# Kernel optimization log

Measured on AMD Instinct MI355X. Metric: run time of the kernel, lower is better.

Reference implementation:

```python
import jax, jax.numpy as jnp
import numpy as np

N = 50000       # nodes
E = 800000      # edges (before self-loops)
F_IN = 128      # num_features
HID = 32        # hidden_dim per head
HEADS = 8
C = 40          # num_classes
NEG_SLOPE = 0.2 # PyG GATConv default leaky_relu slope


def setup_inputs() -> dict:
    key = jax.random.key(0)
    ks = jax.random.split(key, 10)
    x = jax.random.normal(ks[0], (N, F_IN), jnp.float32)
    edge_index = jax.random.randint(ks[1], (2, E), 0, N, dtype=jnp.int64)
    W1 = jax.random.normal(ks[2], (F_IN, HEADS * HID), jnp.float32) * np.float32(1.0 / np.sqrt(F_IN))
    a1_src = jax.random.normal(ks[3], (HEADS, HID), jnp.float32) * 0.1
    a1_dst = jax.random.normal(ks[4], (HEADS, HID), jnp.float32) * 0.1
    b1 = jnp.zeros((HEADS * HID,), jnp.float32)
    W2 = jax.random.normal(ks[5], (HEADS * HID, C), jnp.float32) * np.float32(1.0 / np.sqrt(HEADS * HID))
    a2_src = jax.random.normal(ks[6], (1, C), jnp.float32) * 0.1
    a2_dst = jax.random.normal(ks[7], (1, C), jnp.float32) * 0.1
    b2 = jnp.zeros((C,), jnp.float32)
    return {"x": x, "edge_index": edge_index,
            "W1": W1, "a1_src": a1_src, "a1_dst": a1_dst, "b1": b1,
            "W2": W2, "a2_src": a2_src, "a2_dst": a2_dst, "b2": b2}


def gat_conv(x, edge_index, W, a_src, a_dst, bias):
    """PyG-style GATConv (concat heads, add_self_loops=True), inference mode (no dropout)."""
    n = x.shape[0]
    heads, out_dim = a_src.shape
    ar = jnp.arange(n, dtype=edge_index.dtype)
    src = jnp.concatenate([edge_index[0], ar])   # [E+N]
    dst = jnp.concatenate([edge_index[1], ar])   # [E+N]
    h = (x @ W).reshape(n, heads, out_dim)       # [N, H, D]
    alpha_src = jnp.einsum('nhd,hd->nh', h, a_src)  # [N, H]
    alpha_dst = jnp.einsum('nhd,hd->nh', h, a_dst)  # [N, H]
    e = jax.nn.leaky_relu(alpha_src[src] + alpha_dst[dst], NEG_SLOPE)  # [E+N, H]
    # segment softmax over edges grouped by destination node
    m = jax.ops.segment_max(e, dst, num_segments=n)          # [N, H]
    ex = jnp.exp(e - m[dst])                                  # [E+N, H]
    s = jax.ops.segment_sum(ex, dst, num_segments=n)          # [N, H]
    alpha = ex / (s[dst] + 1e-16)                              # [E+N, H]
    msg = h[src] * alpha[..., None]                            # [E+N, H, D]
    out = jax.ops.segment_sum(msg, dst, num_segments=n)       # [N, H, D]
    return out.reshape(n, heads * out_dim) + bias


def reference(x, edge_index, W1, a1_src, a1_dst, b1, W2, a2_src, a2_dst, b2):
    h = jax.nn.elu(gat_conv(x, edge_index, W1, a1_src, a1_dst, b1))
    # F.dropout is identity in eval mode
    return gat_conv(h, edge_index, W2, a2_src, a2_dst, b2)
```

## Files before the change

kernel.cpp:

```cpp
#include <hip/hip_runtime.h>
#include <math.h>

#define F_IN 128
#define HID 32
#define HEADS 8
#define HD 256
#define NC 40
#define NCP 48
#define H2S 64
#define NEG 0.2f

typedef _Float16 half8 __attribute__((ext_vector_type(8)));
typedef _Float16 half4v __attribute__((ext_vector_type(4)));
typedef float f32x4 __attribute__((ext_vector_type(4)));

__device__ __forceinline__ float leaky(float v) { return v > 0.0f ? v : NEG * v; }
__device__ __forceinline__ float2 up2(unsigned int u) {
    union { unsigned int u; _Float16 h[2]; } c; c.u = u;
    return make_float2((float)c.h[0], (float)c.h[1]);
}

__global__ __launch_bounds__(256) void prep_count_k(const float* __restrict__ W1,
        const float* __restrict__ W2, const float* __restrict__ a1s,
        const float* __restrict__ a1d, _Float16* __restrict__ W1t,
        _Float16* __restrict__ W2t, _Float16* __restrict__ Pt,
        const int* __restrict__ ei, int* __restrict__ deg,
        int* __restrict__ ord, int E) {
    int i = blockIdx.x * 256 + threadIdx.x;
    if (i < HD * F_IN) {
        int c = i >> 7, k = i & 127;
        W1t[i] = (_Float16)W1[k * HD + c];
    }
    int j = i - HD * F_IN;
    if (j >= 0 && j < NCP * HD) {
        int c = j >> 8, k = j & 255;
        W2t[j] = (c < NC) ? (_Float16)W2[k * NC + c] : (_Float16)0.0f;
    }
    int e = i - (HD * F_IN + NCP * HD);
    if (e >= 0 && e < E) {
        int dst = ei[E + e];
        ord[e] = atomicAdd(&deg[dst], 1);
    }
    int p = i - (HD * F_IN + NCP * HD + E);
    if (p >= 0 && p < 16 * F_IN) {
        int pj = p >> 7, k = p & 127;
        int h = pj & 7;
        const float* av = (pj < 8) ? (a1s + h * HID) : (a1d + h * HID);
        const float* wr = W1 + (size_t)k * HD + h * HID;
        float acc = 0.0f;
#pragma unroll 8
        for (int d = 0; d < HID; ++d) acc = fmaf(wr[d], av[d], acc);
        Pt[pj * F_IN + k] = (_Float16)acc;
    }
}

__global__ __launch_bounds__(256) void scan1_k(const int* __restrict__ deg,
        int* __restrict__ rowptr, int* __restrict__ partial, int N) {
    __shared__ int tmp[256];
    int t = threadIdx.x;
    int idx = blockIdx.x * 256 + t;
    int v = (idx < N) ? (deg[idx] + 1) : 0;
    tmp[t] = v;
    __syncthreads();
#pragma unroll
    for (int off = 1; off < 256; off <<= 1) {
        int add = (t >= off) ? tmp[t - off] : 0;
        __syncthreads();
        tmp[t] += add;
        __syncthreads();
    }
    if (idx < N) rowptr[idx] = tmp[t] - v;
    if (t == 255) partial[blockIdx.x] = tmp[255];
}

__global__ __launch_bounds__(256) void scan2_k(int* __restrict__ partial, int P) {
    __shared__ int tmp[256];
    int t = threadIdx.x;
    int v = (t < P) ? partial[t] : 0;
    tmp[t] = v;
    __syncthreads();
#pragma unroll
    for (int off = 1; off < 256; off <<= 1) {
        int add = (t >= off) ? tmp[t - off] : 0;
        __syncthreads();
        tmp[t] += add;
        __syncthreads();
    }
    if (t < P) partial[t] = tmp[t] - v;
}

__global__ __launch_bounds__(256) void scan3_k(int* __restrict__ rowptr,
        const int* __restrict__ partial, int* __restrict__ esrc, int N, int EN) {
    int idx = blockIdx.x * 256 + threadIdx.x;
    if (idx >= N) return;
    int rp = rowptr[idx] + partial[blockIdx.x];
    rowptr[idx] = rp;
    esrc[rp] = idx;
    if (idx == 0) rowptr[N] = EN;
}

__global__ __launch_bounds__(256) void scatter_k(const int* __restrict__ ei,
        const int* __restrict__ rowptr, const int* __restrict__ ord,
        int* __restrict__ esrc, int E) {
    int e = blockIdx.x * 256 + threadIdx.x;
    if (e >= E) return;
    int src = ei[e], dst = ei[E + e];
    esrc[rowptr[dst] + 1 + ord[e]] = src;
}

__global__ __launch_bounds__(256) void gemm1_k(const float* __restrict__ x,
        const _Float16* __restrict__ W1t, const _Float16* __restrict__ Pt,
        _Float16* __restrict__ H1, float* __restrict__ asrc,
        float* __restrict__ adst, int N) {
    int t = threadIdx.x;
    int w = t >> 6, l = t & 63;
    int quad = l >> 4, lr = l & 15;
    int rowA = blockIdx.x * 64 + w * 16 + lr;
    int rowL = rowA < N ? rowA : N - 1;

    half8 af[4];
    const float* xr = x + (size_t)rowL * F_IN + quad * 8;
#pragma unroll
    for (int s = 0; s < 4; ++s) {
        float4 u = *(const float4*)(xr + s * 32);
        float4 v = *(const float4*)(xr + s * 32 + 4);
        half8 a;
        a[0] = (_Float16)u.x; a[1] = (_Float16)u.y;
        a[2] = (_Float16)u.z; a[3] = (_Float16)u.w;
        a[4] = (_Float16)v.x; a[5] = (_Float16)v.y;
        a[6] = (_Float16)v.z; a[7] = (_Float16)v.w;
        af[s] = a;
    }

    int rowC0 = blockIdx.x * 64 + w * 16 + quad * 4;
#pragma unroll
    for (int tt = 0; tt < 16; ++tt) {
        f32x4 acc = {0.0f, 0.0f, 0.0f, 0.0f};
        const _Float16* wp = W1t + (size_t)(tt * 16 + lr) * F_IN + quad * 8;
#pragma unroll
        for (int s = 0; s < 4; ++s) {
            half8 b = *(const half8*)(wp + s * 32);
            acc = __builtin_amdgcn_mfma_f32_16x16x32_f16(af[s], b, acc, 0, 0, 0);
        }
#pragma unroll
        for (int r = 0; r < 4; ++r) {
            int rr = rowC0 + r;
            if (rr < N) H1[(size_t)rr * HD + tt * 16 + lr] = (_Float16)acc[r];
        }
    }
    {
        f32x4 acc = {0.0f, 0.0f, 0.0f, 0.0f};
        const _Float16* pp = Pt + (size_t)lr * F_IN + quad * 8;
#pragma unroll
        for (int s = 0; s < 4; ++s) {
            half8 b = *(const half8*)(pp + s * 32);
            acc = __builtin_amdgcn_mfma_f32_16x16x32_f16(af[s], b, acc, 0, 0, 0);
        }
#pragma unroll
        for (int r = 0; r < 4; ++r) {
            int rr = rowC0 + r;
            if (rr < N) {
                if (lr < 8) asrc[rr * HEADS + lr] = acc[r];
                else        adst[rr * HEADS + (lr - 8)] = acc[r];
            }
        }
    }
}

__global__ __launch_bounds__(256) void agg1_k(const int* __restrict__ esrc,
        const int* __restrict__ rowptr, const float* __restrict__ asrc,
        const float* __restrict__ adst, const _Float16* __restrict__ H1,
        const float* __restrict__ b1, _Float16* __restrict__ out1, int N) {
    int t = threadIdx.x;
    int lane = t & 63;
    int dst = blockIdx.x * 4 + (t >> 6);
    if (dst >= N) return;
    int j = lane & 7;
    int h = lane >> 3;
    int start = rowptr[dst], end = rowptr[dst + 1];
    float adh = adst[dst * HEADS + h];

    float s = 0.0f;
    for (int e = start + j; e < end; e += 8)
        s += __expf(leaky(asrc[esrc[e] * HEADS + h] + adh));
    s += __shfl_xor(s, 1, 64);
    s += __shfl_xor(s, 2, 64);
    s += __shfl_xor(s, 4, 64);
    float inv = 1.0f / (s + 1e-16f);

    float a0 = 0.0f, a1 = 0.0f, a2 = 0.0f, a3 = 0.0f;
    int e = start;
    for (; e + 7 < end; e += 8) {
        int si[8]; float al[8]; uint2 hv[8];
#pragma unroll
        for (int q = 0; q < 8; ++q) si[q] = esrc[e + q];
#pragma unroll
        for (int q = 0; q < 8; ++q) {
            al[q] = asrc[si[q] * HEADS + h];
            hv[q] = *(const uint2*)(H1 + (size_t)si[q] * HD + lane * 4);
        }
#pragma unroll
        for (int q = 0; q < 8; ++q) {
            float w = __expf(leaky(al[q] + adh)) * inv;
            float2 p0 = up2(hv[q].x), p1 = up2(hv[q].y);
            a0 = fmaf(p0.x, w, a0); a1 = fmaf(p0.y, w, a1);
            a2 = fmaf(p1.x, w, a2); a3 = fmaf(p1.y, w, a3);
        }
    }
    for (; e + 3 < end; e += 4) {
        int si[4]; float al[4]; uint2 hv[4];
#pragma unroll
        for (int q = 0; q < 4; ++q) si[q] = esrc[e + q];
#pragma unroll
        for (int q = 0; q < 4; ++q) {
            al[q] = asrc[si[q] * HEADS + h];
            hv[q] = *(const uint2*)(H1 + (size_t)si[q] * HD + lane * 4);
        }
#pragma unroll
        for (int q = 0; q < 4; ++q) {
            float w = __expf(leaky(al[q] + adh)) * inv;
            float2 p0 = up2(hv[q].x), p1 = up2(hv[q].y);
            a0 = fmaf(p0.x, w, a0); a1 = fmaf(p0.y, w, a1);
            a2 = fmaf(p1.x, w, a2); a3 = fmaf(p1.y, w, a3);
        }
    }
    for (; e < end; ++e) {
        int s0 = esrc[e];
        float al0 = asrc[s0 * HEADS + h];
        uint2 h0 = *(const uint2*)(H1 + (size_t)s0 * HD + lane * 4);
        float w0 = __expf(leaky(al0 + adh)) * inv;
        float2 p0 = up2(h0.x), p1 = up2(h0.y);
        a0 = fmaf(p0.x, w0, a0); a1 = fmaf(p0.y, w0, a1);
        a2 = fmaf(p1.x, w0, a2); a3 = fmaf(p1.y, w0, a3);
    }
    float4 bv = *(const float4*)(b1 + lane * 4);
    float o0 = a0 + bv.x, o1 = a1 + bv.y, o2 = a2 + bv.z, o3 = a3 + bv.w;
    o0 = o0 > 0.0f ? o0 : expm1f(o0);
    o1 = o1 > 0.0f ? o1 : expm1f(o1);
    o2 = o2 > 0.0f ? o2 : expm1f(o2);
    o3 = o3 > 0.0f ? o3 : expm1f(o3);
    half4v o;
    o[0] = (_Float16)o0; o[1] = (_Float16)o1;
    o[2] = (_Float16)o2; o[3] = (_Float16)o3;
    *(half4v*)(out1 + (size_t)dst * HD + lane * 4) = o;
}

__global__ __launch_bounds__(256) void gemm2_k(const _Float16* __restrict__ out1,
        const _Float16* __restrict__ W2t, const float* __restrict__ a2s,
        const float* __restrict__ a2d, _Float16* __restrict__ H2h,
        float* __restrict__ asrc2, float* __restrict__ adst2, int N) {
    int t = threadIdx.x;
    int w = t >> 6, l = t & 63;
    int quad = l >> 4, lr = l & 15;
    int rowA = blockIdx.x * 64 + w * 16 + lr;
    int rowL = rowA < N ? rowA : N - 1;

    half8 af[8];
    const _Float16* ar = out1 + (size_t)rowL * HD + quad * 8;
#pragma unroll
    for (int s = 0; s < 8; ++s) af[s] = *(const half8*)(ar + s * 32);

    f32x4 acc[3];
#pragma unroll
    for (int tt = 0; tt < 3; ++tt) {
        f32x4 a = {0.0f, 0.0f, 0.0f, 0.0f};
        const _Float16* wp = W2t + (size_t)(tt * 16 + lr) * HD + quad * 8;
#pragma unroll
        for (int s = 0; s < 8; ++s) {
            half8 b = *(const half8*)(wp + s * 32);
            a = __builtin_amdgcn_mfma_f32_16x16x32_f16(af[s], b, a, 0, 0, 0);
        }
        acc[tt] = a;
    }

    float a2sv[3], a2dv[3];
#pragma unroll
    for (int tt = 0; tt < 3; ++tt) {
        int col = tt * 16 + lr;
        a2sv[tt] = (col < NC) ? a2s[col] : 0.0f;
        a2dv[tt] = (col < NC) ? a2d[col] : 0.0f;
    }
    int rowC0 = blockIdx.x * 64 + w * 16 + quad * 4;
#pragma unroll
    for (int r = 0; r < 4; ++r) {
        int row = rowC0 + r;
        if (row >= N) break;
        float ps = 0.0f, pd = 0.0f;
#pragma unroll
        for (int tt = 0; tt < 3; ++tt) {
            int col = tt * 16 + lr;
            float v = acc[tt][r];
            H2h[(size_t)row * H2S + col] = (_Float16)v;
            ps = fmaf(v, a2sv[tt], ps);
            pd = fmaf(v, a2dv[tt], pd);
        }
        ps += __shfl_xor(ps, 1, 64); ps += __shfl_xor(ps, 2, 64);
        ps += __shfl_xor(ps, 4, 64); ps += __shfl_xor(ps, 8, 64);
        pd += __shfl_xor(pd, 1, 64); pd += __shfl_xor(pd, 2, 64);
        pd += __shfl_xor(pd, 4, 64); pd += __shfl_xor(pd, 8, 64);
        if (lr == 0) { asrc2[row] = ps; adst2[row] = pd; }
    }
}

__global__ __launch_bounds__(256) void agg2_k(const int* __restrict__ esrc,
        const int* __restrict__ rowptr, const float* __restrict__ asrc,
        const float* __restrict__ adst, const _Float16* __restrict__ H2h,
        const float* __restrict__ b2, float* __restrict__ dout, int N) {
    int t = threadIdx.x;
    int g = t >> 6, lane = t & 63;
    int dst = blockIdx.x * 4 + g;
    if (dst >= N) return;
    int start = rowptr[dst], end = rowptr[dst + 1];
    float adst_v = adst[dst];

    float sloc = 0.0f;
    for (int e = start + lane; e < end; e += 64)
        sloc += __expf(leaky(asrc[esrc[e]] + adst_v));
#pragma unroll
    for (int off = 32; off > 0; off >>= 1)
        sloc += __shfl_xor(sloc, off, 64);
    float inv = 1.0f / (sloc + 1e-16f);

    float acc = 0.0f;
    int e = start;
    for (; e + 3 < end; e += 4) {
        int s0 = esrc[e], s1 = esrc[e + 1], s2 = esrc[e + 2], s3 = esrc[e + 3];
        float al0 = asrc[s0], al1 = asrc[s1], al2 = asrc[s2], al3 = asrc[s3];
        float v0 = (float)H2h[(size_t)s0 * H2S + lane];
        float v1 = (float)H2h[(size_t)s1 * H2S + lane];
        float v2 = (float)H2h[(size_t)s2 * H2S + lane];
        float v3 = (float)H2h[(size_t)s3 * H2S + lane];
        float w0 = __expf(leaky(al0 + adst_v)) * inv;
        float w1 = __expf(leaky(al1 + adst_v)) * inv;
        float w2 = __expf(leaky(al2 + adst_v)) * inv;
        float w3 = __expf(leaky(al3 + adst_v)) * inv;
        acc = fmaf(v0, w0, acc);
        acc = fmaf(v1, w1, acc);
        acc = fmaf(v2, w2, acc);
        acc = fmaf(v3, w3, acc);
    }
    for (; e < end; ++e) {
        int s0 = esrc[e];
        float w0 = __expf(leaky(asrc[s0] + adst_v)) * inv;
        acc = fmaf((float)H2h[(size_t)s0 * H2S + lane], w0, acc);
    }
    if (lane < NC) dout[(size_t)dst * NC + lane] = acc + b2[lane];
}

extern "C" void kernel_launch(void* const* d_in, const int* in_sizes, int n_in,
                              void* d_out, int out_size, void* d_ws, size_t ws_size,
                              hipStream_t stream) {
    const float* x   = (const float*)d_in[0];
    const int*   ei  = (const int*)d_in[1];
    const float* W1  = (const float*)d_in[2];
    const float* a1s = (const float*)d_in[3];
    const float* a1d = (const float*)d_in[4];
    const float* b1  = (const float*)d_in[5];
    const float* W2  = (const float*)d_in[6];
    const float* a2s = (const float*)d_in[7];
    const float* a2d = (const float*)d_in[8];
    const float* b2  = (const float*)d_in[9];
    float* dout = (float*)d_out;

    int N = in_sizes[0] / F_IN;
    int E = in_sizes[1] / 2;
    int EN = E + N;
    int NB = (N + 255) / 256;

    char* base = (char*)d_ws;
    size_t off = 0;
    auto carve = [&](size_t bytes) { char* p = base + off; off += (bytes + 255) & ~(size_t)255; return p; };
    _Float16* H1   = (_Float16*)carve((size_t)N * HD * 2);
    _Float16* W1t  = (_Float16*)carve((size_t)HD * F_IN * 2);
    _Float16* W2t  = (_Float16*)carve((size_t)NCP * HD * 2);
    _Float16* Pt   = (_Float16*)carve((size_t)16 * F_IN * 2);
    _Float16* out1 = (_Float16*)carve((size_t)N * HD * 2);
    _Float16* H2h  = (_Float16*)carve((size_t)N * H2S * 2);
    float* asrc1  = (float*)carve((size_t)N * HEADS * 4);
    float* adst1  = (float*)carve((size_t)N * HEADS * 4);
    float* asrc2  = (float*)carve((size_t)N * 4);
    float* adst2  = (float*)carve((size_t)N * 4);
    int*   deg    = (int*)carve((size_t)N * 4);
    int*   ord    = (int*)carve((size_t)E * 4);
    int*   rowptr = (int*)carve((size_t)(N + 1) * 4);
    int*   part   = (int*)carve((size_t)NB * 4);
    int*   esrc   = (int*)carve((size_t)EN * 4);

    hipMemsetAsync(deg, 0, (size_t)N * 4, stream);
    int prep_total = HD * F_IN + NCP * HD + E + 16 * F_IN;
    hipLaunchKernelGGL(prep_count_k, dim3((prep_total + 255) / 256), dim3(256), 0, stream,
                       W1, W2, a1s, a1d, W1t, W2t, Pt, ei, deg, ord, E);
    hipLaunchKernelGGL(scan1_k, dim3(NB), dim3(256), 0, stream, deg, rowptr, part, N);
    hipLaunchKernelGGL(scan2_k, dim3(1), dim3(256), 0, stream, part, NB);
    hipLaunchKernelGGL(scan3_k, dim3(NB), dim3(256), 0, stream, rowptr, part, esrc, N, EN);
    hipLaunchKernelGGL(scatter_k, dim3((E + 255) / 256), dim3(256), 0, stream, ei, rowptr, ord, esrc, E);

    hipLaunchKernelGGL(gemm1_k, dim3((N + 63) / 64), dim3(256), 0, stream,
                       x, W1t, Pt, H1, asrc1, adst1, N);
    hipLaunchKernelGGL(agg1_k, dim3((N + 3) / 4), dim3(256), 0, stream,
                       esrc, rowptr, asrc1, adst1, H1, b1, out1, N);

    hipLaunchKernelGGL(gemm2_k, dim3((N + 63) / 64), dim3(256), 0, stream,
                       out1, W2t, a2s, a2d, H2h, asrc2, adst2, N);
    hipLaunchKernelGGL(agg2_k, dim3((N + 3) / 4), dim3(256), 0, stream,
                       esrc, rowptr, asrc2, adst2, H2h, b2, dout, N);
}
```

Baseline: 316.6 us.

## Fuse softmax denominator into aggregation pass and merge scan kernels

Both aggregation kernels now accumulate the softmax denominator during the single gather pass and normalize once at the end. This removes the separate pass that re-read edge indices and source scores. The second and third scan kernels are merged: every block redundantly scans the partial sums in shared memory, which saves one launch. Layer 2 aggregation also gains an 8-way unrolled gather loop to expose more memory-level parallelism, at the cost of more registers.

```diff
diff --git a/kernel.cpp b/kernel.cpp
--- a/kernel.cpp
+++ b/kernel.cpp
@@ -73,29 +73,27 @@
     if (t == 255) partial[blockIdx.x] = tmp[255];
 }
 
-__global__ __launch_bounds__(256) void scan2_k(int* __restrict__ partial, int P) {
-    __shared__ int tmp[256];
-    int t = threadIdx.x;
-    int v = (t < P) ? partial[t] : 0;
-    tmp[t] = v;
+__global__ __launch_bounds__(256) void scan23_k(int* __restrict__ rowptr,
+        const int* __restrict__ partial, int* __restrict__ esrc,
+        int N, int EN, int NB) {
+    __shared__ int ps[256];
+    int t = threadIdx.x;
+    ps[t] = (t < NB) ? partial[t] : 0;
     __syncthreads();
 #pragma unroll
     for (int off = 1; off < 256; off <<= 1) {
-        int add = (t >= off) ? tmp[t - off] : 0;
+        int add = (t >= off) ? ps[t - off] : 0;
         __syncthreads();
-        tmp[t] += add;
+        ps[t] += add;
         __syncthreads();
     }
-    if (t < P) partial[t] = tmp[t] - v;
-}
-
-__global__ __launch_bounds__(256) void scan3_k(int* __restrict__ rowptr,
-        const int* __restrict__ partial, int* __restrict__ esrc, int N, int EN) {
-    int idx = blockIdx.x * 256 + threadIdx.x;
-    if (idx >= N) return;
-    int rp = rowptr[idx] + partial[blockIdx.x];
-    rowptr[idx] = rp;
-    esrc[rp] = idx;
+    int base = (blockIdx.x == 0) ? 0 : ps[blockIdx.x - 1];
+    int idx = blockIdx.x * 256 + t;
+    if (idx < N) {
+        int rp = rowptr[idx] + base;
+        rowptr[idx] = rp;
+        esrc[rp] = idx;
+    }
     if (idx == 0) rowptr[N] = EN;
 }
 
@@ -175,19 +173,11 @@
     int lane = t & 63;
     int dst = blockIdx.x * 4 + (t >> 6);
     if (dst >= N) return;
-    int j = lane & 7;
     int h = lane >> 3;
     int start = rowptr[dst], end = rowptr[dst + 1];
     float adh = adst[dst * HEADS + h];
 
     float s = 0.0f;
-    for (int e = start + j; e < end; e += 8)
-        s += __expf(leaky(asrc[esrc[e] * HEADS + h] + adh));
-    s += __shfl_xor(s, 1, 64);
-    s += __shfl_xor(s, 2, 64);
-    s += __shfl_xor(s, 4, 64);
-    float inv = 1.0f / (s + 1e-16f);
-
     float a0 = 0.0f, a1 = 0.0f, a2 = 0.0f, a3 = 0.0f;
     int e = start;
     for (; e + 7 < end; e += 8) {
@@ -201,7 +191,8 @@
         }
 #pragma unroll
         for (int q = 0; q < 8; ++q) {
-            float w = __expf(leaky(al[q] + adh)) * inv;
+            float w = __expf(leaky(al[q] + adh));
+            s += w;
             float2 p0 = up2(hv[q].x), p1 = up2(hv[q].y);
             a0 = fmaf(p0.x, w, a0); a1 = fmaf(p0.y, w, a1);
             a2 = fmaf(p1.x, w, a2); a3 = fmaf(p1.y, w, a3);
@@ -218,7 +209,8 @@
         }
 #pragma unroll
         for (int q = 0; q < 4; ++q) {
-            float w = __expf(leaky(al[q] + adh)) * inv;
+            float w = __expf(leaky(al[q] + adh));
+            s += w;
             float2 p0 = up2(hv[q].x), p1 = up2(hv[q].y);
             a0 = fmaf(p0.x, w, a0); a1 = fmaf(p0.y, w, a1);
             a2 = fmaf(p1.x, w, a2); a3 = fmaf(p1.y, w, a3);
@@ -228,13 +220,16 @@
         int s0 = esrc[e];
         float al0 = asrc[s0 * HEADS + h];
         uint2 h0 = *(const uint2*)(H1 + (size_t)s0 * HD + lane * 4);
-        float w0 = __expf(leaky(al0 + adh)) * inv;
+        float w0 = __expf(leaky(al0 + adh));
+        s += w0;
         float2 p0 = up2(h0.x), p1 = up2(h0.y);
         a0 = fmaf(p0.x, w0, a0); a1 = fmaf(p0.y, w0, a1);
         a2 = fmaf(p1.x, w0, a2); a3 = fmaf(p1.y, w0, a3);
     }
+    float inv = 1.0f / (s + 1e-16f);
     float4 bv = *(const float4*)(b1 + lane * 4);
-    float o0 = a0 + bv.x, o1 = a1 + bv.y, o2 = a2 + bv.z, o3 = a3 + bv.w;
+    float o0 = fmaf(a0, inv, bv.x), o1 = fmaf(a1, inv, bv.y);
+    float o2 = fmaf(a2, inv, bv.z), o3 = fmaf(a3, inv, bv.w);
     o0 = o0 > 0.0f ? o0 : expm1f(o0);
     o1 = o1 > 0.0f ? o1 : expm1f(o1);
     o2 = o2 > 0.0f ? o2 : expm1f(o2);
@@ -313,38 +308,48 @@
     int start = rowptr[dst], end = rowptr[dst + 1];
     float adst_v = adst[dst];
 
-    float sloc = 0.0f;
-    for (int e = start + lane; e < end; e += 64)
-        sloc += __expf(leaky(asrc[esrc[e]] + adst_v));
-#pragma unroll
-    for (int off = 32; off > 0; off >>= 1)
-        sloc += __shfl_xor(sloc, off, 64);
-    float inv = 1.0f / (sloc + 1e-16f);
-
+    float s = 0.0f;
     float acc = 0.0f;
     int e = start;
+    for (; e + 7 < end; e += 8) {
+        int si[8]; float al[8]; float v[8];
+#pragma unroll
+        for (int q = 0; q < 8; ++q) si[q] = esrc[e + q];
+#pragma unroll
+        for (int q = 0; q < 8; ++q) {
+            al[q] = asrc[si[q]];
+            v[q] = (float)H2h[(size_t)si[q] * H2S + lane];
+        }
+#pragma unroll
+        for (int q = 0; q < 8; ++q) {
+            float w = __expf(leaky(al[q] + adst_v));
+            s += w;
+            acc = fmaf(v[q], w, acc);
+        }
+    }
     for (; e + 3 < end; e += 4) {
-        int s0 = esrc[e], s1 = esrc[e + 1], s2 = esrc[e + 2], s3 = esrc[e + 3];
-        float al0 = asrc[s0], al1 = asrc[s1], al2 = asrc[s2], al3 = asrc[s3];
-        float v0 = (float)H2h[(size_t)s0 * H2S + lane];
-        float v1 = (float)H2h[(size_t)s1 * H2S + lane];
-        float v2 = (float)H2h[(size_t)s2 * H2S + lane];
-        float v3 = (float)H2h[(size_t)s3 * H2S + lane];
-        float w0 = __expf(leaky(al0 + adst_v)) * inv;
-        float w1 = __expf(leaky(al1 + adst_v)) * inv;
-        float w2 = __expf(leaky(al2 + adst_v)) * inv;
-        float w3 = __expf(leaky(al3 + adst_v)) * inv;
-        acc = fmaf(v0, w0, acc);
-        acc = fmaf(v1, w1, acc);
-        acc = fmaf(v2, w2, acc);
-        acc = fmaf(v3, w3, acc);
+        int si[4]; float al[4]; float v[4];
+#pragma unroll
+        for (int q = 0; q < 4; ++q) si[q] = esrc[e + q];
+#pragma unroll
+        for (int q = 0; q < 4; ++q) {
+            al[q] = asrc[si[q]];
+            v[q] = (float)H2h[(size_t)si[q] * H2S + lane];
+        }
+#pragma unroll
+        for (int q = 0; q < 4; ++q) {
+            float w = __expf(leaky(al[q] + adst_v));
+            s += w;
+            acc = fmaf(v[q], w, acc);
+        }
     }
     for (; e < end; ++e) {
         int s0 = esrc[e];
-        float w0 = __expf(leaky(asrc[s0] + adst_v)) * inv;
+        float w0 = __expf(leaky(asrc[s0] + adst_v));
+        s += w0;
         acc = fmaf((float)H2h[(size_t)s0 * H2S + lane], w0, acc);
     }
-    if (lane < NC) dout[(size_t)dst * NC + lane] = acc + b2[lane];
+    if (lane < NC) dout[(size_t)dst * NC + lane] = acc / (s + 1e-16f) + b2[lane];
 }
 
 extern "C" void kernel_launch(void* const* d_in, const int* in_sizes, int n_in,
@@ -391,8 +396,7 @@
     hipLaunchKernelGGL(prep_count_k, dim3((prep_total + 255) / 256), dim3(256), 0, stream,
                        W1, W2, a1s, a1d, W1t, W2t, Pt, ei, deg, ord, E);
     hipLaunchKernelGGL(scan1_k, dim3(NB), dim3(256), 0, stream, deg, rowptr, part, N);
-    hipLaunchKernelGGL(scan2_k, dim3(1), dim3(256), 0, stream, part, NB);
-    hipLaunchKernelGGL(scan3_k, dim3(NB), dim3(256), 0, stream, rowptr, part, esrc, N, EN);
+    hipLaunchKernelGGL(scan23_k, dim3(NB), dim3(256), 0, stream, rowptr, part, esrc, N, EN, NB);
     hipLaunchKernelGGL(scatter_k, dim3((E + 255) / 256), dim3(256), 0, stream, ei, rowptr, ord, esrc, E);
 
     hipLaunchKernelGGL(gemm1_k, dim3((N + 63) / 64), dim3(256), 0, stream,
```

Result: faster. 294.6 us (-6.9%).
